# Optimization experiments

Measured on AMD Instinct MI355X. Metric: run time of the kernel, lower is better.

The kernel has to match this reference:

```python
import jax, jax.numpy as jnp
import numpy as np

# (in_dim, out_dim) for fc1..fc14, hard-coded in the torch module
DIMS = [(12,12),(12,11),(11,10),(10,9),(9,8),(8,7),(7,6),(6,7),(7,8),(8,9),(9,10),(10,11),(11,12),(12,2)]
BATCH = 2_000_000


def setup_inputs() -> dict:
    key = jax.random.key(0)
    keys = jax.random.split(key, 2 * len(DIMS) + 1)
    inp = {"x": jax.random.normal(keys[0], (BATCH, 12), dtype=jnp.float32)}
    for i, (din, dout) in enumerate(DIMS):
        s = 1.0 / np.sqrt(din)  # torch nn.Linear default init range
        inp[f"w{i+1}"] = jax.random.uniform(keys[2*i+1], (dout, din), jnp.float32, -s, s)
        inp[f"b{i+1}"] = jax.random.uniform(keys[2*i+2], (dout,), jnp.float32, -s, s)
    return inp


def _forward(x, Ws, Bs):
    lin = lambda h, i: h @ Ws[i].T + Bs[i]
    # encoder half: fc1..fc6 with ReLU, saving identities 1..6
    ids = []
    h = x
    for i in range(6):
        h = jax.nn.relu(lin(h, i))
        ids.append(h)
    # bottleneck fc7
    h = jax.nn.relu(lin(h, 6))
    # decoder half: fc8..fc13, each adds the matching identity before ReLU
    # fc8 (+id6), fc9 (+id5), ..., fc13 (+id1)
    for i in range(7, 13):
        h = jax.nn.relu(lin(h, i) + ids[12 - i])
    # fc14 + softmax over class dim
    return jax.nn.softmax(lin(h, 13), axis=1)


def reference(x, w1, b1, w2, b2, w3, b3, w4, b4, w5, b5, w6, b6, w7, b7,
              w8, b8, w9, b9, w10, b10, w11, b11, w12, b12, w13, b13, w14, b14):
    Ws = [w1, w2, w3, w4, w5, w6, w7, w8, w9, w10, w11, w12, w13, w14]
    Bs = [b1, b2, b3, b4, b5, b6, b7, b8, b9, b10, b11, b12, b13, b14]
    return _forward(x, Ws, Bs)
```

## Files before the change

### kernel.cpp

```cpp
#include <hip/hip_runtime.h>
#include <math.h>

#define DEV __device__ __forceinline__

typedef float f2 __attribute__((ext_vector_type(2)));

DEV f2 splat(float s) { f2 r; r.x = s; r.y = s; return r; }

template <int DIN, int DOUT>
DEV void lin2(const float* __restrict__ w, const float* __restrict__ b,
              const f2* in, f2* out) {
#pragma unroll
    for (int o = 0; o < DOUT; ++o) out[o] = splat(b[o]);
#pragma unroll
    for (int k = 0; k < DIN; ++k) {
        f2 xk = in[k];
#pragma unroll
        for (int o = 0; o < DOUT; ++o)
            out[o] = __builtin_elementwise_fma(xk, splat(w[o * DIN + k]), out[o]);
    }
}

template <int DIN, int DOUT>
DEV void lin2_skip(const float* __restrict__ w, const float* __restrict__ b,
                   const f2* in, const f2* skip, f2* out) {
#pragma unroll
    for (int o = 0; o < DOUT; ++o) out[o] = splat(b[o]) + skip[o];
#pragma unroll
    for (int k = 0; k < DIN; ++k) {
        f2 xk = in[k];
#pragma unroll
        for (int o = 0; o < DOUT; ++o)
            out[o] = __builtin_elementwise_fma(xk, splat(w[o * DIN + k]), out[o]);
    }
}

template <int N>
DEV void relu_ip(f2* v) {
#pragma unroll
    for (int k = 0; k < N; ++k) v[k] = __builtin_elementwise_max(v[k], splat(0.0f));
}

__global__ void __launch_bounds__(256, 2)
csnet14_kernel(const float* __restrict__ x,
               const float* __restrict__ w1,  const float* __restrict__ b1,
               const float* __restrict__ w2,  const float* __restrict__ b2,
               const float* __restrict__ w3,  const float* __restrict__ b3,
               const float* __restrict__ w4,  const float* __restrict__ b4,
               const float* __restrict__ w5,  const float* __restrict__ b5,
               const float* __restrict__ w6,  const float* __restrict__ b6,
               const float* __restrict__ w7,  const float* __restrict__ b7,
               const float* __restrict__ w8,  const float* __restrict__ b8,
               const float* __restrict__ w9,  const float* __restrict__ b9,
               const float* __restrict__ w10, const float* __restrict__ b10,
               const float* __restrict__ w11, const float* __restrict__ b11,
               const float* __restrict__ w12, const float* __restrict__ b12,
               const float* __restrict__ w13, const float* __restrict__ b13,
               const float* __restrict__ w14, const float* __restrict__ b14,
               float* __restrict__ out, int nt) {
    int t = blockIdx.x * blockDim.x + threadIdx.x;
    if (t >= nt) return;

    const float4* xr = reinterpret_cast<const float4*>(x + (size_t)t * 24);
    float4 a0 = xr[0], a1 = xr[1], a2 = xr[2];
    float4 a3 = xr[3], a4 = xr[4], a5 = xr[5];
    float r0[12] = {a0.x, a0.y, a0.z, a0.w, a1.x, a1.y, a1.z, a1.w,
                    a2.x, a2.y, a2.z, a2.w};
    float r1[12] = {a3.x, a3.y, a3.z, a3.w, a4.x, a4.y, a4.z, a4.w,
                    a5.x, a5.y, a5.z, a5.w};
    f2 h0[12];
#pragma unroll
    for (int k = 0; k < 12; ++k) { h0[k].x = r0[k]; h0[k].y = r1[k]; }

    f2 id1[12]; lin2<12, 12>(w1, b1, h0,  id1); relu_ip<12>(id1);
    f2 id2[11]; lin2<12, 11>(w2, b2, id1, id2); relu_ip<11>(id2);
    f2 id3[10]; lin2<11, 10>(w3, b3, id2, id3); relu_ip<10>(id3);
    f2 id4[9];  lin2<10,  9>(w4, b4, id3, id4); relu_ip<9>(id4);
    f2 id5[8];  lin2< 9,  8>(w5, b5, id4, id5); relu_ip<8>(id5);
    f2 id6[7];  lin2< 8,  7>(w6, b6, id5, id6); relu_ip<7>(id6);

    f2 t7[6];   lin2< 7,  6>(w7, b7, id6, t7);  relu_ip<6>(t7);

    f2 t8[7];   lin2_skip< 6,  7>(w8,  b8,  t7,  id6, t8);  relu_ip<7>(t8);
    f2 t9[8];   lin2_skip< 7,  8>(w9,  b9,  t8,  id5, t9);  relu_ip<8>(t9);
    f2 t10[9];  lin2_skip< 8,  9>(w10, b10, t9,  id4, t10); relu_ip<9>(t10);
    f2 t11[10]; lin2_skip< 9, 10>(w11, b11, t10, id3, t11); relu_ip<10>(t11);
    f2 t12[11]; lin2_skip<10, 11>(w12, b12, t11, id2, t12); relu_ip<11>(t12);
    f2 t13[12]; lin2_skip<11, 12>(w13, b13, t12, id1, t13); relu_ip<12>(t13);

    f2 l[2];    lin2<12,  2>(w14, b14, t13, l);
    f2 m  = __builtin_elementwise_max(l[0], l[1]);
    f2 d0 = l[0] - m;
    f2 d1 = l[1] - m;
    float e0a = __expf(d0.x), e0b = __expf(d0.y);
    float e1a = __expf(d1.x), e1b = __expf(d1.y);
    float inva = __builtin_amdgcn_rcpf(e0a + e1a);
    float invb = __builtin_amdgcn_rcpf(e0b + e1b);

    float4 o;
    o.x = e0a * inva;
    o.y = e1a * inva;
    o.z = e0b * invb;
    o.w = e1b * invb;
    reinterpret_cast<float4*>(out)[t] = o;
}

extern "C" void kernel_launch(void* const* d_in, const int* in_sizes, int n_in,
                              void* d_out, int out_size, void* d_ws, size_t ws_size,
                              hipStream_t stream) {
    const float* x   = (const float*)d_in[0];
    const float* w1  = (const float*)d_in[1];  const float* b1  = (const float*)d_in[2];
    const float* w2  = (const float*)d_in[3];  const float* b2  = (const float*)d_in[4];
    const float* w3  = (const float*)d_in[5];  const float* b3  = (const float*)d_in[6];
    const float* w4  = (const float*)d_in[7];  const float* b4  = (const float*)d_in[8];
    const float* w5  = (const float*)d_in[9];  const float* b5  = (const float*)d_in[10];
    const float* w6  = (const float*)d_in[11]; const float* b6  = (const float*)d_in[12];
    const float* w7  = (const float*)d_in[13]; const float* b7  = (const float*)d_in[14];
    const float* w8  = (const float*)d_in[15]; const float* b8  = (const float*)d_in[16];
    const float* w9  = (const float*)d_in[17]; const float* b9  = (const float*)d_in[18];
    const float* w10 = (const float*)d_in[19]; const float* b10 = (const float*)d_in[20];
    const float* w11 = (const float*)d_in[21]; const float* b11 = (const float*)d_in[22];
    const float* w12 = (const float*)d_in[23]; const float* b12 = (const float*)d_in[24];
    const float* w13 = (const float*)d_in[25]; const float* b13 = (const float*)d_in[26];
    const float* w14 = (const float*)d_in[27]; const float* b14 = (const float*)d_in[28];
    float* out = (float*)d_out;

    const int n  = in_sizes[0] / 12;
    const int nt = n / 2;
    dim3 block(256);
    dim3 grid((nt + 255) / 256);
    csnet14_kernel<<<grid, block, 0, stream>>>(
        x, w1, b1, w2, b2, w3, b3, w4, b4, w5, b5, w6, b6, w7, b7,
        w8, b8, w9, b9, w10, b10, w11, b11, w12, b12, w13, b13, w14, b14,
        out, nt);
}
```

Baseline: 229.2 us.

## Process one row per thread with scalar FMAs instead of packed row pairs

Replaces the two-rows-per-thread packed float2 FMA formulation with one row per thread using scalar FMAs, and doubles the grid accordingly. Raises the launch-bounds occupancy hint from 2 to 4 blocks. The intent is to cut register pressure and raise occupancy, at the cost of losing packed FP32 math, which issues two FMAs per instruction. Global loads and stores become narrower per thread.

```diff
diff --git a/kernel.cpp b/kernel.cpp
--- a/kernel.cpp
+++ b/kernel.cpp
@@ -3,45 +3,41 @@
 
 #define DEV __device__ __forceinline__
 
-typedef float f2 __attribute__((ext_vector_type(2)));
-
-DEV f2 splat(float s) { f2 r; r.x = s; r.y = s; return r; }
-
 template <int DIN, int DOUT>
-DEV void lin2(const float* __restrict__ w, const float* __restrict__ b,
-              const f2* in, f2* out) {
+DEV void lin(const float* __restrict__ w, const float* __restrict__ b,
+             const float* in, float* out) {
 #pragma unroll
-    for (int o = 0; o < DOUT; ++o) out[o] = splat(b[o]);
+    for (int o = 0; o < DOUT; ++o) out[o] = b[o];
 #pragma unroll
     for (int k = 0; k < DIN; ++k) {
-        f2 xk = in[k];
+        float xk = in[k];
 #pragma unroll
         for (int o = 0; o < DOUT; ++o)
-            out[o] = __builtin_elementwise_fma(xk, splat(w[o * DIN + k]), out[o]);
+            out[o] = __builtin_fmaf(xk, w[o * DIN + k], out[o]);
     }
 }
 
 template <int DIN, int DOUT>
-DEV void lin2_skip(const float* __restrict__ w, const float* __restrict__ b,
-                   const f2* in, const f2* skip, f2* out) {
+DEV void lin_skip(const float* __restrict__ w, const float* __restrict__ b,
+                  const float* in, const float* skip, float* out) {
 #pragma unroll
-    for (int o = 0; o < DOUT; ++o) out[o] = splat(b[o]) + skip[o];
+    for (int o = 0; o < DOUT; ++o) out[o] = b[o] + skip[o];
 #pragma unroll
     for (int k = 0; k < DIN; ++k) {
-        f2 xk = in[k];
+        float xk = in[k];
 #pragma unroll
         for (int o = 0; o < DOUT; ++o)
-            out[o] = __builtin_elementwise_fma(xk, splat(w[o * DIN + k]), out[o]);
+            out[o] = __builtin_fmaf(xk, w[o * DIN + k], out[o]);
     }
 }
 
 template <int N>
-DEV void relu_ip(f2* v) {
+DEV void relu_ip(float* v) {
 #pragma unroll
-    for (int k = 0; k < N; ++k) v[k] = __builtin_elementwise_max(v[k], splat(0.0f));
+    for (int k = 0; k < N; ++k) v[k] = fmaxf(v[k], 0.0f);
 }
 
-__global__ void __launch_bounds__(256, 2)
+__global__ void __launch_bounds__(256, 4)
 csnet14_kernel(const float* __restrict__ x,
                const float* __restrict__ w1,  const float* __restrict__ b1,
                const float* __restrict__ w2,  const float* __restrict__ b2,
@@ -57,52 +53,41 @@
                const float* __restrict__ w12, const float* __restrict__ b12,
                const float* __restrict__ w13, const float* __restrict__ b13,
                const float* __restrict__ w14, const float* __restrict__ b14,
-               float* __restrict__ out, int nt) {
+               float* __restrict__ out, int n) {
     int t = blockIdx.x * blockDim.x + threadIdx.x;
-    if (t >= nt) return;
+    if (t >= n) return;
 
-    const float4* xr = reinterpret_cast<const float4*>(x + (size_t)t * 24);
+    const float4* xr = reinterpret_cast<const float4*>(x + (size_t)t * 12);
     float4 a0 = xr[0], a1 = xr[1], a2 = xr[2];
-    float4 a3 = xr[3], a4 = xr[4], a5 = xr[5];
-    float r0[12] = {a0.x, a0.y, a0.z, a0.w, a1.x, a1.y, a1.z, a1.w,
+    float h0[12] = {a0.x, a0.y, a0.z, a0.w, a1.x, a1.y, a1.z, a1.w,
                     a2.x, a2.y, a2.z, a2.w};
-    float r1[12] = {a3.x, a3.y, a3.z, a3.w, a4.x, a4.y, a4.z, a4.w,
-                    a5.x, a5.y, a5.z, a5.w};
-    f2 h0[12];
-#pragma unroll
-    for (int k = 0; k < 12; ++k) { h0[k].x = r0[k]; h0[k].y = r1[k]; }
 
-    f2 id1[12]; lin2<12, 12>(w1, b1, h0,  id1); relu_ip<12>(id1);
-    f2 id2[11]; lin2<12, 11>(w2, b2, id1, id2); relu_ip<11>(id2);
-    f2 id3[10]; lin2<11, 10>(w3, b3, id2, id3); relu_ip<10>(id3);
-    f2 id4[9];  lin2<10,  9>(w4, b4, id3, id4); relu_ip<9>(id4);
-    f2 id5[8];  lin2< 9,  8>(w5, b5, id4, id5); relu_ip<8>(id5);
-    f2 id6[7];  lin2< 8,  7>(w6, b6, id5, id6); relu_ip<7>(id6);
+    float id1[12]; lin<12, 12>(w1, b1, h0,  id1); relu_ip<12>(id1);
+    float id2[11]; lin<12, 11>(w2, b2, id1, id2); relu_ip<11>(id2);
+    float id3[10]; lin<11, 10>(w3, b3, id2, id3); relu_ip<10>(id3);
+    float id4[9];  lin<10,  9>(w4, b4, id3, id4); relu_ip<9>(id4);
+    float id5[8];  lin< 9,  8>(w5, b5, id4, id5); relu_ip<8>(id5);
+    float id6[7];  lin< 8,  7>(w6, b6, id5, id6); relu_ip<7>(id6);
 
-    f2 t7[6];   lin2< 7,  6>(w7, b7, id6, t7);  relu_ip<6>(t7);
+    float t7[6];   lin< 7,  6>(w7, b7, id6, t7);  relu_ip<6>(t7);
 
-    f2 t8[7];   lin2_skip< 6,  7>(w8,  b8,  t7,  id6, t8);  relu_ip<7>(t8);
-    f2 t9[8];   lin2_skip< 7,  8>(w9,  b9,  t8,  id5, t9);  relu_ip<8>(t9);
-    f2 t10[9];  lin2_skip< 8,  9>(w10, b10, t9,  id4, t10); relu_ip<9>(t10);
-    f2 t11[10]; lin2_skip< 9, 10>(w11, b11, t10, id3, t11); relu_ip<10>(t11);
-    f2 t12[11]; lin2_skip<10, 11>(w12, b12, t11, id2, t12); relu_ip<11>(t12);
-    f2 t13[12]; lin2_skip<11, 12>(w13, b13, t12, id1, t13); relu_ip<12>(t13);
+    float t8[7];   lin_skip< 6,  7>(w8,  b8,  t7,  id6, t8);  relu_ip<7>(t8);
+    float t9[8];   lin_skip< 7,  8>(w9,  b9,  t8,  id5, t9);  relu_ip<8>(t9);
+    float t10[9];  lin_skip< 8,  9>(w10, b10, t9,  id4, t10); relu_ip<9>(t10);
+    float t11[10]; lin_skip< 9, 10>(w11, b11, t10, id3, t11); relu_ip<10>(t11);
+    float t12[11]; lin_skip<10, 11>(w12, b12, t11, id2, t12); relu_ip<11>(t12);
+    float t13[12]; lin_skip<11, 12>(w13, b13, t12, id1, t13); relu_ip<12>(t13);
 
-    f2 l[2];    lin2<12,  2>(w14, b14, t13, l);
-    f2 m  = __builtin_elementwise_max(l[0], l[1]);
-    f2 d0 = l[0] - m;
-    f2 d1 = l[1] - m;
-    float e0a = __expf(d0.x), e0b = __expf(d0.y);
-    float e1a = __expf(d1.x), e1b = __expf(d1.y);
-    float inva = __builtin_amdgcn_rcpf(e0a + e1a);
-    float invb = __builtin_amdgcn_rcpf(e0b + e1b);
+    float l[2];    lin<12,  2>(w14, b14, t13, l);
+    float m  = fmaxf(l[0], l[1]);
+    float e0 = __expf(l[0] - m);
+    float e1 = __expf(l[1] - m);
+    float inv = __builtin_amdgcn_rcpf(e0 + e1);
 
-    float4 o;
-    o.x = e0a * inva;
-    o.y = e1a * inva;
-    o.z = e0b * invb;
-    o.w = e1b * invb;
-    reinterpret_cast<float4*>(out)[t] = o;
+    float2 o;
+    o.x = e0 * inv;
+    o.y = e1 * inv;
+    reinterpret_cast<float2*>(out)[t] = o;
 }
 
 extern "C" void kernel_launch(void* const* d_in, const int* in_sizes, int n_in,
@@ -125,12 +110,11 @@
     const float* w14 = (const float*)d_in[27]; const float* b14 = (const float*)d_in[28];
     float* out = (float*)d_out;
 
-    const int n  = in_sizes[0] / 12;
-    const int nt = n / 2;
+    const int n = in_sizes[0] / 12;
     dim3 block(256);
-    dim3 grid((nt + 255) / 256);
+    dim3 grid((n + 255) / 256);
     csnet14_kernel<<<grid, block, 0, stream>>>(
         x, w1, b1, w2, b2, w3, b3, w4, b4, w5, b5, w6, b6, w7, b7,
         w8, b8, w9, b9, w10, b10, w11, b11, w12, b12, w13, b13, w14, b14,
-        out, nt);
+        out, n);
 }
```

Result: slower. 242.6 us (+5.9%).
